# Kernel tuning notes

Hardware: AMD Instinct MI355X
Metric: run time of the kernel (lower is better)

Reference implementation:

```python
import jax, jax.numpy as jnp
import numpy as np

OUT_CHN, IN_CHN, K = 256, 256, 3
STRIDE, PADDING = 1, 1

def binary_activation(x):
    # STE: forward = sign(x), backward = piecewise-polynomial surrogate out3
    m1 = (x < -1).astype(x.dtype)
    m2 = (x < 0).astype(x.dtype)
    m3 = (x < 1).astype(x.dtype)
    out1 = -1.0 * m1 + (x * x + 2 * x) * (1 - m1)
    out2 = out1 * m2 + (-x * x + 2 * x) * (1 - m2)
    out3 = out2 * m3 + 1.0 * (1 - m3)
    return jax.lax.stop_gradient(jnp.sign(x)) - jax.lax.stop_gradient(out3) + out3

def setup_inputs() -> dict:
    key = jax.random.key(0)
    kx, kw = jax.random.split(key)
    x = jax.random.normal(kx, (32, IN_CHN, 56, 56), dtype=jnp.float32)
    # weights stored flat [N,1] as in the torch module, scaled by 0.001
    weights = jax.random.uniform(kw, (OUT_CHN * IN_CHN * K * K, 1), dtype=jnp.float32) * 0.001
    return {"x": x, "weights": weights}

def reference(x, weights):
    w = weights.reshape(OUT_CHN, IN_CHN, K, K)
    # STE for weights: forward = sign(w), backward = clamp(w,-1,1)
    clipped = jnp.clip(w, -1.0, 1.0)
    bw = jax.lax.stop_gradient(jnp.sign(w)) - jax.lax.stop_gradient(clipped) + clipped
    bx = binary_activation(x)
    y = jax.lax.conv_general_dilated(
        bx, bw,
        window_strides=(STRIDE, STRIDE),
        padding=[(PADDING, PADDING), (PADDING, PADDING)],
        dimension_numbers=("NCHW", "OIHW", "NCHW"),
    )
    return y
```

## Files before the change

kernel.cpp:

```cpp
#include <hip/hip_runtime.h>
#include <stdint.h>

#define N_BATCH 32
#define CHN     256
#define HW      56
#define HP      58
#define HPT     7

#define XPAD_CELLS (N_BATCH * HP * 2 * HP)
#define XPAD_U32   (XPAD_CELLS * 4)

__global__ __launch_bounds__(256) void prep_kernel(const float* __restrict__ x,
                                                   const float* __restrict__ wsrc,
                                                   uint32_t* __restrict__ xpad,
                                                   uint32_t* __restrict__ wbits,
                                                   int* __restrict__ wpop) {
    __shared__ int part[9][4];
    int bid  = blockIdx.x;
    int t    = threadIdx.x;
    int lane = t & 63;

    if (bid < 784) {
        int tid = bid * 256 + t;
        int n   = tid / 6272;
        int rem = tid - n * 6272;
        int hf  = rem / 3136;
        int pq  = rem - hf * 3136;

        const float* src = x + ((size_t)(n * 256 + hf * 128)) * 3136 + pq;
        uint32_t b0 = 0, b1 = 0, b2 = 0, b3 = 0;
#pragma unroll
        for (int g = 0; g < 8; g++) {
            float v[16];
#pragma unroll
            for (int i = 0; i < 16; i++) v[i] = src[(size_t)(g * 16 + i) * 3136];
#pragma unroll
            for (int i = 0; i < 16; i++) {
                int c = g * 16 + i;
                uint32_t b = v[i] > 0.0f ? 1u : 0u;
                if ((c >> 5) == 0) b0 |= b << (c & 31);
                else if ((c >> 5) == 1) b1 |= b << (c & 31);
                else if ((c >> 5) == 2) b2 |= b << (c & 31);
                else b3 |= b << (c & 31);
            }
        }
        int h = pq / 56;
        int w = pq - h * 56;
        uint32_t cell = ((uint32_t)(n * HP + h + 1) * 2 + hf) * HP + (w + 1);
        ((uint4*)xpad)[cell] = make_uint4(b0, b1, b2, b3);
    } else if (bid < 841) {
        int u = (bid - 784) * 256 + t;
        if (u < 14592) {
            int p = u / 228;
            int e = u - p * 228;
            int n = p >> 1, h = p & 1;
            int hp, wp;
            if (e < 58)       { hp = 0;       wp = e;       }
            else if (e < 116) { hp = 57;      wp = e - 58;  }
            else if (e < 172) { hp = e - 115; wp = 0;       }
            else              { hp = e - 171; wp = 57;      }
            uint32_t cell = ((uint32_t)(n * HP + hp) * 2 + h) * HP + wp;
            ((uint4*)xpad)[cell] = make_uint4(0u, 0u, 0u, 0u);
        }
    } else {
        int o  = bid - 841;
        int wv = t >> 6;
        const float* p = wsrc + ((size_t)o * 256 + t) * 9;
        float v[9];
#pragma unroll
        for (int tap = 0; tap < 9; tap++) v[tap] = p[tap];
#pragma unroll
        for (int tap = 0; tap < 9; tap++) {
            unsigned long long m = __ballot(v[tap] > 0.0f);
            if (lane == 0) {
                wbits[(size_t)(o * 9 + tap) * 8 + 2 * wv]     = (uint32_t)m;
                wbits[(size_t)(o * 9 + tap) * 8 + 2 * wv + 1] = (uint32_t)(m >> 32);
                part[tap][wv] = __builtin_popcountll(m);
            }
        }
        __syncthreads();
        if (t < 9) wpop[o * 9 + t] = part[t][0] + part[t][1] + part[t][2] + part[t][3];
    }
}

__global__ __launch_bounds__(256) void conv_kernel(const uint32_t* __restrict__ xpad,
                                                   const uint32_t* __restrict__ wbits,
                                                   const int* __restrict__ wpop,
                                                   float* __restrict__ out) {
    __shared__ uint4 sx[1044];

    int t     = threadIdx.x;
    int lane  = t & 63;
    int wv    = t >> 6;
    int strip = blockIdx.x;
    int og    = blockIdx.y;
    int n     = blockIdx.z;
    int hb    = strip * HPT;

    const uint4* xg = (const uint4*)xpad + (size_t)(n * HP + hb) * (2 * HP);
    for (int i = t; i < 1044; i += 256)
        sx[i] = xg[i];
    __syncthreads();

    const char* sxb = (const char*)sx + lane * 16;

#pragma unroll 1
    for (int oi = 0; oi < 4; oi++) {
        int o = __builtin_amdgcn_readfirstlane(og * 16 + wv * 4 + oi);
        const uint32_t* wa = wbits + (size_t)o * 72;

        uint32_t W[72];
#pragma unroll
        for (int i = 0; i < 72; i++) W[i] = wa[i];

        int acc[HPT];
#pragma unroll
        for (int r = 0; r < HPT; r++) acc[r] = 0;

#pragma unroll
        for (int j = 0; j < HPT + 2; j++) {
            uint4 X0a = *(const uint4*)(sxb + ((j * 2 + 0) * HP + 0) * 16);
            uint4 X1a = *(const uint4*)(sxb + ((j * 2 + 0) * HP + 1) * 16);
            uint4 X2a = *(const uint4*)(sxb + ((j * 2 + 0) * HP + 2) * 16);
            uint4 X0b = *(const uint4*)(sxb + ((j * 2 + 1) * HP + 0) * 16);
            uint4 X1b = *(const uint4*)(sxb + ((j * 2 + 1) * HP + 1) * 16);
            uint4 X2b = *(const uint4*)(sxb + ((j * 2 + 1) * HP + 2) * 16);
#pragma unroll
            for (int dh = 0; dh < 3; dh++) {
                int r = j - dh;
                if (r >= 0 && r < HPT) {
#pragma unroll
                    for (int dw = 0; dw < 3; dw++) {
                        uint4 Xa = (dw == 0) ? X0a : (dw == 1) ? X1a : X2a;
                        uint4 Xb = (dw == 0) ? X0b : (dw == 1) ? X1b : X2b;
                        int ta = (dh * 3 + dw) * 8;
                        acc[r] += __builtin_popcount(Xa.x ^ W[ta + 0])
                                + __builtin_popcount(Xa.y ^ W[ta + 1])
                                + __builtin_popcount(Xa.z ^ W[ta + 2])
                                + __builtin_popcount(Xa.w ^ W[ta + 3])
                                + __builtin_popcount(Xb.x ^ W[ta + 4])
                                + __builtin_popcount(Xb.y ^ W[ta + 5])
                                + __builtin_popcount(Xb.z ^ W[ta + 6])
                                + __builtin_popcount(Xb.w ^ W[ta + 7]);
                    }
                }
            }
        }

        if (lane < 56) {
            int w = lane;
            const int* wpa = wpop + (size_t)o * 9;
            int pa[9];
#pragma unroll
            for (int tp = 0; tp < 9; tp++) pa[tp] = wpa[tp];
            float* oa = out + (((size_t)n * 256 + o) * 56 + hb) * 56 + w;
            bool edge_w = (w == 0) | (w == 55);
#pragma unroll
            for (int r = 0; r < HPT; r++) {
                int hh = hb + r;
                int va = 2304 - 2 * acc[r];
                if (edge_w | (hh == 0) | (hh == 55)) {
                    int ca = 0;
#pragma unroll
                    for (int dh = -1; dh <= 1; dh++)
#pragma unroll
                        for (int dw = -1; dw <= 1; dw++)
                            if ((unsigned)(hh + dh) >= 56u || (unsigned)(w + dw) >= 56u)
                                ca += 256 - 2 * pa[(dh + 1) * 3 + (dw + 1)];
                    va -= ca;
                }
                oa[(size_t)r * 56] = (float)va;
            }
        }
    }
}

extern "C" void kernel_launch(void* const* d_in, const int* in_sizes, int n_in,
                              void* d_out, int out_size, void* d_ws, size_t ws_size,
                              hipStream_t stream) {
    const float* x    = (const float*)d_in[0];
    const float* wsrc = (const float*)d_in[1];
    float* out = (float*)d_out;

    uint32_t* xpad  = (uint32_t*)d_ws;
    uint32_t* wbits = xpad + XPAD_U32;
    int*      wpop  = (int*)(wbits + 256 * 9 * 8);

    prep_kernel<<<1097, 256, 0, stream>>>(x, wsrc, xpad, wbits, wpop);
    conv_kernel<<<dim3(8, 16, N_BATCH), 256, 0, stream>>>(xpad, wbits, wpop, out);
}
```

Before: 359.4 us.

## Remap conv so each lane owns an output channel, stage outputs in LDS

```diff
diff --git a/kernel.cpp b/kernel.cpp
--- a/kernel.cpp
+++ b/kernel.cpp
@@ -5,7 +5,6 @@
 #define CHN     256
 #define HW      56
 #define HP      58
-#define HPT     7
 
 #define XPAD_CELLS (N_BATCH * HP * 2 * HP)
 #define XPAD_U32   (XPAD_CELLS * 4)
@@ -83,95 +82,77 @@
     }
 }
 
-__global__ __launch_bounds__(256) void conv_kernel(const uint32_t* __restrict__ xpad,
-                                                   const uint32_t* __restrict__ wbits,
-                                                   const int* __restrict__ wpop,
-                                                   float* __restrict__ out) {
-    __shared__ uint4 sx[1044];
+__global__ __launch_bounds__(256, 2)
+void conv_kernel(const uint32_t* __restrict__ xpad,
+                 const uint32_t* __restrict__ wbits,
+                 const int* __restrict__ wpop,
+                 float* __restrict__ out) {
+    __shared__ uint4 sx[3 * 2 * HP];
+    __shared__ float obuf[4 * 64 * 57];
 
-    int t     = threadIdx.x;
-    int lane  = t & 63;
-    int wv    = t >> 6;
-    int strip = blockIdx.x;
-    int og    = blockIdx.y;
-    int n     = blockIdx.z;
-    int hb    = strip * HPT;
+    int t    = threadIdx.x;
+    int lane = t & 63;
+    int wv   = t >> 6;
+    int h    = blockIdx.x;
+    int n    = blockIdx.y;
 
-    const uint4* xg = (const uint4*)xpad + (size_t)(n * HP + hb) * (2 * HP);
-    for (int i = t; i < 1044; i += 256)
-        sx[i] = xg[i];
+    const uint4* xg = (const uint4*)xpad + ((size_t)n * HP + h) * (2 * HP);
+    for (int i = t; i < 3 * 2 * HP; i += 256) sx[i] = xg[i];
+
+    int o = wv * 64 + lane;
+    const uint4* wsrc4 = (const uint4*)(wbits + (size_t)o * 72);
+    uint4 W4[18];
+#pragma unroll
+    for (int i = 0; i < 18; i++) W4[i] = wsrc4[i];
+
+    const int* wpa = wpop + (size_t)o * 9;
+    int pa[9];
+#pragma unroll
+    for (int i = 0; i < 9; i++) pa[i] = wpa[i];
+
     __syncthreads();
 
-    const char* sxb = (const char*)sx + lane * 16;
+    float* ob = obuf + wv * (64 * 57);
+    bool hedge = (h == 0) | (h == 55);
 
-#pragma unroll 1
-    for (int oi = 0; oi < 4; oi++) {
-        int o = __builtin_amdgcn_readfirstlane(og * 16 + wv * 4 + oi);
-        const uint32_t* wa = wbits + (size_t)o * 72;
+#pragma unroll 2
+    for (int w = 0; w < 56; w++) {
+        const uint4* cb = sx + w;
+        int a0 = 0, a1 = 0, a2 = 0, a3 = 0;
+#pragma unroll
+        for (int r = 0; r < 3; r++)
+#pragma unroll
+            for (int dw = 0; dw < 3; dw++)
+#pragma unroll
+                for (int hf = 0; hf < 2; hf++) {
+                    uint4 Xc = cb[(r * 2 + hf) * HP + dw];
+                    uint4 Wc = W4[(r * 3 + dw) * 2 + hf];
+                    a0 += __builtin_popcount(Xc.x ^ Wc.x);
+                    a1 += __builtin_popcount(Xc.y ^ Wc.y);
+                    a2 += __builtin_popcount(Xc.z ^ Wc.z);
+                    a3 += __builtin_popcount(Xc.w ^ Wc.w);
+                }
+        int va = 2304 - 2 * ((a0 + a1) + (a2 + a3));
+        if (hedge | (w == 0) | (w == 55)) {
+            int ca = 0;
+#pragma unroll
+            for (int dh = 0; dh < 3; dh++)
+#pragma unroll
+                for (int dw = 0; dw < 3; dw++)
+                    if ((unsigned)(h + dh - 1) >= 56u || (unsigned)(w + dw - 1) >= 56u)
+                        ca += 256 - 2 * pa[dh * 3 + dw];
+            va -= ca;
+        }
+        ob[lane * 57 + w] = (float)va;
+    }
 
-        uint32_t W[72];
-#pragma unroll
-        for (int i = 0; i < 72; i++) W[i] = wa[i];
+    __syncthreads();
 
-        int acc[HPT];
-#pragma unroll
-        for (int r = 0; r < HPT; r++) acc[r] = 0;
-
-#pragma unroll
-        for (int j = 0; j < HPT + 2; j++) {
-            uint4 X0a = *(const uint4*)(sxb + ((j * 2 + 0) * HP + 0) * 16);
-            uint4 X1a = *(const uint4*)(sxb + ((j * 2 + 0) * HP + 1) * 16);
-            uint4 X2a = *(const uint4*)(sxb + ((j * 2 + 0) * HP + 2) * 16);
-            uint4 X0b = *(const uint4*)(sxb + ((j * 2 + 1) * HP + 0) * 16);
-            uint4 X1b = *(const uint4*)(sxb + ((j * 2 + 1) * HP + 1) * 16);
-            uint4 X2b = *(const uint4*)(sxb + ((j * 2 + 1) * HP + 2) * 16);
-#pragma unroll
-            for (int dh = 0; dh < 3; dh++) {
-                int r = j - dh;
-                if (r >= 0 && r < HPT) {
-#pragma unroll
-                    for (int dw = 0; dw < 3; dw++) {
-                        uint4 Xa = (dw == 0) ? X0a : (dw == 1) ? X1a : X2a;
-                        uint4 Xb = (dw == 0) ? X0b : (dw == 1) ? X1b : X2b;
-                        int ta = (dh * 3 + dw) * 8;
-                        acc[r] += __builtin_popcount(Xa.x ^ W[ta + 0])
-                                + __builtin_popcount(Xa.y ^ W[ta + 1])
-                                + __builtin_popcount(Xa.z ^ W[ta + 2])
-                                + __builtin_popcount(Xa.w ^ W[ta + 3])
-                                + __builtin_popcount(Xb.x ^ W[ta + 4])
-                                + __builtin_popcount(Xb.y ^ W[ta + 5])
-                                + __builtin_popcount(Xb.z ^ W[ta + 6])
-                                + __builtin_popcount(Xb.w ^ W[ta + 7]);
-                    }
-                }
-            }
-        }
-
-        if (lane < 56) {
-            int w = lane;
-            const int* wpa = wpop + (size_t)o * 9;
-            int pa[9];
-#pragma unroll
-            for (int tp = 0; tp < 9; tp++) pa[tp] = wpa[tp];
-            float* oa = out + (((size_t)n * 256 + o) * 56 + hb) * 56 + w;
-            bool edge_w = (w == 0) | (w == 55);
-#pragma unroll
-            for (int r = 0; r < HPT; r++) {
-                int hh = hb + r;
-                int va = 2304 - 2 * acc[r];
-                if (edge_w | (hh == 0) | (hh == 55)) {
-                    int ca = 0;
-#pragma unroll
-                    for (int dh = -1; dh <= 1; dh++)
-#pragma unroll
-                        for (int dw = -1; dw <= 1; dw++)
-                            if ((unsigned)(hh + dh) >= 56u || (unsigned)(w + dw) >= 56u)
-                                ca += 256 - 2 * pa[(dh + 1) * 3 + (dw + 1)];
-                    va -= ca;
-                }
-                oa[(size_t)r * 56] = (float)va;
-            }
-        }
+    if (lane < 56) {
+        float* orow = out + (((size_t)n * 256 + wv * 64) * 56 + h) * 56 + lane;
+#pragma unroll 8
+        for (int o2 = 0; o2 < 64; o2++)
+            orow[(size_t)o2 * 3136] = ob[o2 * 57 + lane];
     }
 }
 
@@ -187,5 +168,5 @@
     int*      wpop  = (int*)(wbits + 256 * 9 * 8);
 
     prep_kernel<<<1097, 256, 0, stream>>>(x, wsrc, xpad, wbits, wpop);
-    conv_kernel<<<dim3(8, 16, N_BATCH), 256, 0, stream>>>(xpad, wbits, wpop, out);
+    conv_kernel<<<dim3(HW, N_BATCH), 256, 0, stream>>>(xpad, wbits, wpop, out);
 }
```

New measurement: 299.9 us. 1.2x faster.
